# Performance work log

Measured on AMD Instinct MI355X. Metric: run time of the kernel, lower is better.

## Reference

```python
import jax, jax.numpy as jnp
import numpy as np
from jax import lax

EPS = 1e-5

def _instance_norm(x):
    # per-sample, per-channel over HW, affine=False (torch default), biased var
    m = jnp.mean(x, axis=(2, 3), keepdims=True)
    v = jnp.mean((x - m) ** 2, axis=(2, 3), keepdims=True)
    return (x - m) / jnp.sqrt(v + EPS)

def _lrelu(x):
    return jax.nn.leaky_relu(x, 0.2)

def _conv(x, w, b, stride=1, pad=0):
    y = lax.conv_general_dilated(x, w, (stride, stride), ((pad, pad), (pad, pad)),
                                 dimension_numbers=('NCHW', 'OIHW', 'NCHW'))
    return y + b[None, :, None, None]

def _conv_transpose(x, w, b):
    # torch ConvTranspose2d(k=3, stride=2, padding=1, output_padding=1)
    # == dilated conv with lhs_dilation=2, pad (k-1-p, k-1-p+op) = (1, 2),
    # kernel spatially flipped and in/out swapped. w: (Cin, Cout, 3, 3)
    wt = jnp.flip(w, axis=(2, 3)).transpose(1, 0, 2, 3)  # (Cout, Cin, 3, 3)
    y = lax.conv_general_dilated(x, wt, (1, 1), ((1, 2), (1, 2)),
                                 lhs_dilation=(2, 2),
                                 dimension_numbers=('NCHW', 'OIHW', 'NCHW'))
    return y + b[None, :, None, None]

def _reflect_pad1(x):
    return jnp.pad(x, ((0, 0), (0, 0), (1, 1), (1, 1)), mode='reflect')

def _nearest_resize(x, out_h, out_w):
    in_h, in_w = x.shape[2], x.shape[3]
    iy = (jnp.arange(out_h) * (in_h / out_h)).astype(jnp.int32)
    ix = (jnp.arange(out_w) * (in_w / out_w)).astype(jnp.int32)
    return x[:, :, iy][:, :, :, ix]

def setup_inputs() -> dict:
    key = jax.random.key(0)
    ks = jax.random.split(key, 12)
    B, S, H, W = 8, 19, 256, 256
    out_nc = 512
    inp = jax.random.normal(ks[0], (B, 3, H, W), dtype=jnp.float32)
    labels = jax.random.randint(ks[1], (B, 1, H, W), 0, S)
    segmap = (labels == jnp.arange(S).reshape(1, S, 1, 1)).astype(jnp.float32)
    sc = 0.05
    return {
        'input': inp, 'segmap': segmap,
        'w1': jax.random.normal(ks[2], (32, 3, 3, 3), jnp.float32) * sc,
        'b1': jnp.zeros((32,), jnp.float32),
        'w2': jax.random.normal(ks[3], (64, 32, 3, 3), jnp.float32) * sc,
        'b2': jnp.zeros((64,), jnp.float32),
        'w3': jax.random.normal(ks[4], (128, 64, 3, 3), jnp.float32) * sc,
        'b3': jnp.zeros((128,), jnp.float32),
        'w4': jax.random.normal(ks[5], (128, 256, 3, 3), jnp.float32) * sc,  # torch convT layout (Cin, Cout, kh, kw)
        'b4': jnp.zeros((256,), jnp.float32),
        'w5': jax.random.normal(ks[6], (out_nc, 256, 3, 3), jnp.float32) * sc,
        'b5': jnp.zeros((out_nc,), jnp.float32),
    }

def _backbone(x, w1, b1, w2, b2, w3, b3, w4, b4, w5, b5):
    x = _lrelu(_instance_norm(_conv(_reflect_pad1(x), w1, b1)))          # [B,32,256,256]
    x = _lrelu(_instance_norm(_conv(x, w2, b2, stride=2, pad=1)))        # [B,64,128,128]
    x = _lrelu(_instance_norm(_conv(x, w3, b3, stride=2, pad=1)))        # [B,128,64,64]
    x = _lrelu(_instance_norm(_conv_transpose(x, w4, b4)))               # [B,256,128,128]
    x = jnp.tanh(_conv(_reflect_pad1(x), w5, b5))                        # [B,512,128,128]
    return x

def reference(input, segmap, w1, b1, w2, b2, w3, b3, w4, b4, w5, b5):
    codes = _backbone(input, w1, b1, w2, b2, w3, b3, w4, b4, w5, b5)
    seg = _nearest_resize(segmap, codes.shape[2], codes.shape[3])
    mask = (seg > 0).astype(codes.dtype)                                  # segmap.bool()
    sums = jnp.einsum('bchw,bshw->bsc', codes, mask)                      # masked sum per (b, class)
    counts = jnp.sum(mask, axis=(2, 3))[:, :, None]                       # [B,S,1]
    return jnp.where(counts > 0, sums / jnp.maximum(counts, 1.0), 0.0)    # [B,S,C]
```

## Files before the change

### kernel.cpp

```cpp
#include <hip/hip_runtime.h>

#define LB __launch_bounds__(256)

constexpr int S = 19;

typedef __attribute__((ext_vector_type(8))) short frag16;
typedef __attribute__((ext_vector_type(8))) ushort ushort8;
typedef __attribute__((ext_vector_type(4))) float f32x4;

__device__ __forceinline__ int reflect256(int i) { return i < 0 ? -i : (i > 255 ? 510 - i : i); }
__device__ __forceinline__ int reflect128(int i) { return i < 0 ? -i : (i > 127 ? 254 - i : i); }

__device__ __forceinline__ ushort f2bf(float f) {
    union { float f; uint u; } a; a.f = f;
    uint r = a.u + 0x7fffu + ((a.u >> 16) & 1u);
    return (ushort)(r >> 16);
}
__device__ __forceinline__ float bf2f(ushort u) {
    union { uint u; float f; } a; a.u = ((uint)u) << 16; return a.f;
}

__device__ __forceinline__ void gll16(const void* g, void* l) {
    __builtin_amdgcn_global_load_lds(
        (const __attribute__((address_space(1))) void*)g,
        (__attribute__((address_space(3))) void*)l, 16, 0, 0);
}

__global__ LB void k_prep(const float* __restrict__ w2, const float* __restrict__ w3,
                          const float* __restrict__ w4, const float* __restrict__ w5,
                          ushort* __restrict__ t2, ushort* __restrict__ t3,
                          ushort* __restrict__ t4, ushort* __restrict__ t5,
                          float* __restrict__ zf, int ZN) {
    int e = blockIdx.x * 256 + threadIdx.x;
    if (e < ZN) zf[e] = 0.f;
    if (e < 18432) {
        int ci = e & 31, co = (e >> 5) & 63, tap = e >> 11;
        t2[e] = f2bf(w2[(co * 32 + ci) * 9 + tap]);
    } else if (e < 18432 + 73728) {
        int e2 = e - 18432;
        int ci = e2 & 63, co = (e2 >> 6) & 127, tap = e2 >> 13;
        t3[e2] = f2bf(w3[(co * 64 + ci) * 9 + tap]);
    } else if (e < 18432 + 73728 + 294912) {
        int e3 = e - (18432 + 73728);
        int ci = e3 & 127, co = (e3 >> 7) & 255, tap = e3 >> 15;
        t4[e3] = f2bf(w4[ci * 2304 + co * 9 + tap]);
    } else {
        int e4 = e - (18432 + 73728 + 294912);
        int ci = e4 & 255, co = (e4 >> 8) & 511, tap = e4 >> 17;
        t5[e4] = f2bf(w5[(co * 256 + ci) * 9 + tap]);
    }
}

__global__ LB void k_conv1cl(const float* __restrict__ in, const float* __restrict__ w,
                             const float* __restrict__ bias, ushort* __restrict__ out) {
    __shared__ float Wr[864];
    __shared__ float Bs[32];
    int t = threadIdx.x;
    for (int e = t; e < 864; e += 256) Wr[e] = w[e];
    if (t < 32) Bs[t] = bias[t];
    __syncthreads();
    int idx = blockIdx.x * 256 + t;
    int x = idx & 255, y = (idx >> 8) & 255, b = idx >> 16;
    float v[27];
    #pragma unroll
    for (int ci = 0; ci < 3; ++ci) {
        const float* ip = in + ((b * 3 + ci) << 16);
        #pragma unroll
        for (int ky = 0; ky < 3; ++ky) {
            int iy = reflect256(y + ky - 1);
            #pragma unroll
            for (int kx = 0; kx < 3; ++kx) {
                int ix = reflect256(x + kx - 1);
                v[ci * 9 + ky * 3 + kx] = ip[(iy << 8) + ix];
            }
        }
    }
    ushort* op = out + (long)idx * 32;
    #pragma unroll
    for (int g = 0; g < 4; ++g) {
        ushort8 o;
        #pragma unroll
        for (int j = 0; j < 8; ++j) {
            int co = g * 8 + j;
            float a = Bs[co];
            #pragma unroll
            for (int k = 0; k < 27; ++k) a += v[k] * Wr[co * 27 + k];
            o[j] = f2bf(a);
        }
        *(ushort8*)(op + g * 8) = o;
    }
}

template <int C, int PB, int SPLITS>
__global__ LB void k_stats_cl(const ushort* __restrict__ x,
                              float* __restrict__ psum, float* __restrict__ pss) {
    __shared__ float lsum[C], lss[C];
    int b = blockIdx.x / SPLITS, sp = blockIdx.x % SPLITS;
    int t = threadIdx.x;
    if (t < C) { lsum[t] = 0.f; lss[t] = 0.f; }
    __syncthreads();
    constexpr int CG = C / 8;
    constexpr int PO = 256 / CG;
    int c0 = (t % CG) * 8;
    int po = t / CG;
    float s[8], ss[8];
    #pragma unroll
    for (int k = 0; k < 8; ++k) { s[k] = 0.f; ss[k] = 0.f; }
    const ushort* base = x + ((long)b * SPLITS + sp) * (long)PB * C;
    for (int p = po; p < PB; p += PO) {
        ushort8 v = *(const ushort8*)(base + (long)p * C + c0);
        #pragma unroll
        for (int k = 0; k < 8; ++k) {
            float f = bf2f(v[k]);
            s[k] += f; ss[k] += f * f;
        }
    }
    #pragma unroll
    for (int k = 0; k < 8; ++k) {
        atomicAdd(&lsum[c0 + k], s[k]);
        atomicAdd(&lss[c0 + k], ss[k]);
    }
    __syncthreads();
    if (t < C) {
        atomicAdd(&psum[b * C + t], lsum[t]);
        atomicAdd(&pss[b * C + t], lss[t]);
    }
}

template <int C, int P>
__global__ LB void k_nl_cl(ushort* __restrict__ x, const float* __restrict__ psum,
                           const float* __restrict__ pss) {
    __shared__ float M[C], I[C];
    int t = threadIdx.x;
    long e0 = (long)blockIdx.x * 2048;
    int b = (int)(e0 / ((long)P * C));
    if (t < C) {
        float s = psum[b * C + t], q = pss[b * C + t];
        float m = s / (float)P;
        float v = q / (float)P - m * m;
        M[t] = m;
        I[t] = rsqrtf(v + 1e-5f);
    }
    __syncthreads();
    long e = e0 + t * 8;
    int c0 = (int)(e % C);
    ushort8 v = *(ushort8*)(x + e);
    #pragma unroll
    for (int k = 0; k < 8; ++k) {
        float u = (bf2f(v[k]) - M[c0 + k]) * I[c0 + k];
        u = u > 0.f ? u : 0.2f * u;
        v[k] = f2bf(u);
    }
    *(ushort8*)(x + e) = v;
}

__global__ LB void k_conv2m(const ushort* __restrict__ xin, const ushort* __restrict__ wt,
                            const float* __restrict__ bias, ushort* __restrict__ xout) {
    int bx = blockIdx.x;
    int y = bx & 127, b = bx >> 7;
    int t = threadIdx.x, w = t >> 6, lane = t & 63;
    int col0 = w * 32;
    int lanep = lane & 15, hi = lane >> 4;

    f32x4 acc[4][2];
    #pragma unroll
    for (int m = 0; m < 4; ++m)
        #pragma unroll
        for (int n = 0; n < 2; ++n) acc[m][n] = (f32x4){0.f, 0.f, 0.f, 0.f};

    #pragma unroll
    for (int ky = 0; ky < 3; ++ky) {
        int iy = 2 * y + ky - 1;
        if (iy < 0) continue;
        #pragma unroll
        for (int kx = 0; kx < 3; ++kx) {
            int tap = ky * 3 + kx;
            const ushort* wb = wt + ((tap * 64 + lanep) << 5) + hi * 8;
            frag16 av[4];
            #pragma unroll
            for (int m = 0; m < 4; ++m) av[m] = *(const frag16*)(wb + ((m * 16) << 5));
            frag16 bv[2];
            #pragma unroll
            for (int n = 0; n < 2; ++n) {
                int xo = col0 + n * 16 + lanep;
                int ix = 2 * xo + kx - 1;
                frag16 vv = (frag16)(short)0;
                if (ix >= 0)
                    vv = *(const frag16*)(xin + ((((long)(b * 256 + iy)) << 8) + ix) * 32 + hi * 8);
                bv[n] = vv;
            }
            #pragma unroll
            for (int m = 0; m < 4; ++m)
                #pragma unroll
                for (int n = 0; n < 2; ++n)
                    acc[m][n] = __builtin_amdgcn_mfma_f32_16x16x32_bf16(av[m], bv[n], acc[m][n], 0, 0, 0);
        }
    }
    float bvv[4][4];
    #pragma unroll
    for (int m = 0; m < 4; ++m)
        #pragma unroll
        for (int r = 0; r < 4; ++r) bvv[m][r] = bias[m * 16 + hi * 4 + r];
    #pragma unroll
    for (int n = 0; n < 2; ++n) {
        int xo = col0 + n * 16 + lanep;
        long pb = ((((long)(b * 128 + y)) << 7) + xo) * 64 + hi * 4;
        #pragma unroll
        for (int m = 0; m < 4; ++m) {
            ushort4 o;
            o.x = f2bf(acc[m][n][0] + bvv[m][0]);
            o.y = f2bf(acc[m][n][1] + bvv[m][1]);
            o.z = f2bf(acc[m][n][2] + bvv[m][2]);
            o.w = f2bf(acc[m][n][3] + bvv[m][3]);
            *(ushort4*)(xout + pb + m * 16) = o;
        }
    }
}

__global__ LB void k_conv3m(const ushort* __restrict__ xin, const ushort* __restrict__ wt,
                            const float* __restrict__ bias, ushort* __restrict__ xout) {
    int bx = blockIdx.x;
    int y = bx & 63, b = bx >> 6;
    int t = threadIdx.x, w = t >> 6, lane = t & 63;
    int co0 = (w >> 1) * 64;
    int col0 = (w & 1) * 32;
    int lanep = lane & 15, hi = lane >> 4;

    f32x4 acc[4][2];
    #pragma unroll
    for (int m = 0; m < 4; ++m)
        #pragma unroll
        for (int n = 0; n < 2; ++n) acc[m][n] = (f32x4){0.f, 0.f, 0.f, 0.f};

    #pragma unroll
    for (int ky = 0; ky < 3; ++ky) {
        int iy = 2 * y + ky - 1;
        if (iy < 0) continue;
        #pragma unroll
        for (int kx = 0; kx < 3; ++kx) {
            int tap = ky * 3 + kx;
            #pragma unroll
            for (int ck = 0; ck < 2; ++ck) {
                int ci0 = ck * 32;
                const ushort* wb = wt + ((tap * 128 + co0 + lanep) << 6) + ci0 + hi * 8;
                frag16 av[4];
                #pragma unroll
                for (int m = 0; m < 4; ++m) av[m] = *(const frag16*)(wb + ((m * 16) << 6));
                frag16 bv[2];
                #pragma unroll
                for (int n = 0; n < 2; ++n) {
                    int xo = col0 + n * 16 + lanep;
                    int ix = 2 * xo + kx - 1;
                    frag16 vv = (frag16)(short)0;
                    if (ix >= 0)
                        vv = *(const frag16*)(xin + ((((long)(b * 128 + iy)) << 7) + ix) * 64 + ci0 + hi * 8);
                    bv[n] = vv;
                }
                #pragma unroll
                for (int m = 0; m < 4; ++m)
                    #pragma unroll
                    for (int n = 0; n < 2; ++n)
                        acc[m][n] = __builtin_amdgcn_mfma_f32_16x16x32_bf16(av[m], bv[n], acc[m][n], 0, 0, 0);
            }
        }
    }
    float bvv[4][4];
    #pragma unroll
    for (int m = 0; m < 4; ++m)
        #pragma unroll
        for (int r = 0; r < 4; ++r) bvv[m][r] = bias[co0 + m * 16 + hi * 4 + r];
    #pragma unroll
    for (int n = 0; n < 2; ++n) {
        int xo = col0 + n * 16 + lanep;
        long pb = ((((long)(b * 64 + y)) << 6) + xo) * 128 + co0 + hi * 4;
        #pragma unroll
        for (int m = 0; m < 4; ++m) {
            ushort4 o;
            o.x = f2bf(acc[m][n][0] + bvv[m][0]);
            o.y = f2bf(acc[m][n][1] + bvv[m][1]);
            o.z = f2bf(acc[m][n][2] + bvv[m][2]);
            o.w = f2bf(acc[m][n][3] + bvv[m][3]);
            *(ushort4*)(xout + pb + m * 16) = o;
        }
    }
}

__global__ LB void k_convt4m(const ushort* __restrict__ x3l, const ushort* __restrict__ wt,
                             const float* __restrict__ bias, ushort* __restrict__ xl) {
    int bx = blockIdx.x;
    int parity = bx & 3;
    int py = parity >> 1, px = parity & 1;
    int rg = (bx >> 2) & 15;
    int ct = (bx >> 6) & 3;
    int b  = bx >> 8;
    int co0 = ct * 64;
    int t = threadIdx.x;
    int w = t >> 6;
    int ip = rg * 4 + w;
    int lane = t & 63;
    int lanep = lane & 15;
    int hi = lane >> 4;
    int laneq = hi * 8;

    f32x4 acc[4][4];
    #pragma unroll
    for (int m = 0; m < 4; ++m)
        #pragma unroll
        for (int n = 0; n < 4; ++n) acc[m][n] = (f32x4){0.f, 0.f, 0.f, 0.f};

    #pragma unroll
    for (int ky = 0; ky < 3; ++ky) {
        if (((ky + py) & 1) == 0) continue;
        int i = ip + ((py == 1 && ky == 0) ? 1 : 0);
        if (i >= 64) continue;
        #pragma unroll
        for (int kx = 0; kx < 3; ++kx) {
            if (((kx + px) & 1) == 0) continue;
            int dxp = (px == 1 && kx == 0) ? 1 : 0;
            int tap = ky * 3 + kx;
            const ushort* wbase = wt + (((long)tap * 256 + co0 + lanep) << 7) + laneq;
            const ushort* xbase = x3l + ((((long)b << 12) + (i << 6)) << 7) + laneq;
            #pragma unroll
            for (int ci0 = 0; ci0 < 128; ci0 += 32) {
                frag16 av[4], bv[4];
                #pragma unroll
                for (int m = 0; m < 4; ++m)
                    av[m] = *(const frag16*)(wbase + ((m * 16) << 7) + ci0);
                #pragma unroll
                for (int n = 0; n < 4; ++n) {
                    int j = n * 16 + lanep + dxp;
                    bool valid = j < 64;
                    frag16 v = *(const frag16*)(xbase + ((valid ? j : 63) << 7) + ci0);
                    if (!valid) v = (frag16)(short)0;
                    bv[n] = v;
                }
                #pragma unroll
                for (int m = 0; m < 4; ++m)
                    #pragma unroll
                    for (int n = 0; n < 4; ++n)
                        acc[m][n] = __builtin_amdgcn_mfma_f32_16x16x32_bf16(av[m], bv[n], acc[m][n], 0, 0, 0);
            }
        }
    }

    float bvv[4][4];
    #pragma unroll
    for (int m = 0; m < 4; ++m)
        #pragma unroll
        for (int r = 0; r < 4; ++r)
            bvv[m][r] = bias[co0 + m * 16 + hi * 4 + r];
    int y = 2 * ip + py;
    #pragma unroll
    for (int n = 0; n < 4; ++n) {
        int x = 2 * (n * 16 + lanep) + px;
        long pb = ((((long)b << 14) + (y << 7) + x) << 8) + co0 + hi * 4;
        #pragma unroll
        for (int m = 0; m < 4; ++m) {
            ushort4 o;
            o.x = f2bf(acc[m][n][0] + bvv[m][0]);
            o.y = f2bf(acc[m][n][1] + bvv[m][1]);
            o.z = f2bf(acc[m][n][2] + bvv[m][2]);
            o.w = f2bf(acc[m][n][3] + bvv[m][3]);
            *(ushort4*)(xl + pb + m * 16) = o;
        }
    }
}

__global__ LB void k_label(const float* __restrict__ segmap, int* __restrict__ lab,
                           int* __restrict__ counts) {
    __shared__ int h[S];
    if (threadIdx.x < S) h[threadIdx.x] = 0;
    __syncthreads();
    int idx = blockIdx.x * 256 + threadIdx.x;
    int x = idx & 127, y = (idx >> 7) & 127, b = idx >> 14;
    const float* sp = segmap + (long)b * S * 65536 + (y << 1) * 256 + (x << 1);
    int s = 0;
    for (int c = 0; c < S; ++c) {
        if (sp[c * 65536] > 0.f) { s = c; break; }
    }
    lab[idx] = s;
    atomicAdd(&h[s], 1);
    __syncthreads();
    if (threadIdx.x < S) atomicAdd(&counts[b * S + threadIdx.x], h[threadIdx.x]);
}

__global__ void __launch_bounds__(256, 2)
k_conv5m(const ushort* __restrict__ xl, const ushort* __restrict__ wt,
         const float* __restrict__ bias, const int* __restrict__ lab,
         float* __restrict__ sumbuf) {
    __shared__ __align__(16) ushort L[35072];
    float* part = (float*)L;
    constexpr int XS = 0, WS = 16640;

    int bx = blockIdx.x;
    int yp = bx & 63;
    int ct = (bx >> 6) & 7;
    int b  = bx >> 9;
    int y0 = yp * 2, cob = ct * 64;
    int t = threadIdx.x;
    int w = t >> 6;
    int lane = t & 63;
    int row_w = w & 1;
    int col0 = (w >> 1) * 64;
    int lanep = lane & 15;
    int hi = lane >> 4;
    int xw8 = (hi ^ ((lanep >> 1) & 3)) * 8;

    long xbase = (long)b << 14;
    long xg[9]; int wg[9];
    #pragma unroll
    for (int k = 0; k < 9; ++k) {
        int e = t + k * 256;
        int q = e & 3, p = e >> 2;
        int qp = q ^ ((p >> 1) & 3);
        if (e < 2080) {
            int r = p / 130, c = p - r * 130;
            int gy = reflect128(y0 - 1 + r);
            int gc = reflect128(c - 1);
            xg[k] = ((xbase + (gy << 7) + gc) << 8) + qp * 8;
        } else xg[k] = xbase << 8;
        wg[k] = (((p >> 6) * 512 + cob + (p & 63)) << 8) + qp * 8;
    }

    f32x4 acc[4][4];
    #pragma unroll
    for (int m = 0; m < 4; ++m)
        #pragma unroll
        for (int n = 0; n < 4; ++n) acc[m][n] = (f32x4){0.f, 0.f, 0.f, 0.f};

    #pragma unroll 1
    for (int c8 = 0; c8 < 8; ++c8) {
        int cin = c8 * 32;
        #pragma unroll
        for (int k = 0; k < 8; ++k) gll16(xl + xg[k] + cin, L + XS + ((k << 8) + t) * 8);
        if (t < 32) gll16(xl + xg[8] + cin, L + XS + ((8 << 8) + t) * 8);
        #pragma unroll
        for (int k = 0; k < 9; ++k) gll16(wt + wg[k] + cin, L + WS + ((k << 8) + t) * 8);
        __syncthreads();
        #pragma unroll
        for (int tap = 0; tap < 9; ++tap) {
            int ky = tap / 3, kx = tap % 3;
            frag16 av[4];
            #pragma unroll
            for (int m = 0; m < 4; ++m)
                av[m] = *(const frag16*)(L + WS + (tap * 64 + m * 16 + lanep) * 32 + xw8);
            int p0 = (row_w + ky) * 130 + col0 + kx + lanep;
            int bo = p0 * 32 + (hi ^ ((p0 >> 1) & 3)) * 8;
            frag16 bf[4];
            #pragma unroll
            for (int n = 0; n < 4; ++n)
                bf[n] = *(const frag16*)(L + XS + bo + n * 512);
            #pragma unroll
            for (int m = 0; m < 4; ++m)
                #pragma unroll
                for (int n = 0; n < 4; ++n)
                    acc[m][n] = __builtin_amdgcn_mfma_f32_16x16x32_bf16(av[m], bf[n], acc[m][n], 0, 0, 0);
        }
        __syncthreads();
    }

    float bv[4][4];
    #pragma unroll
    for (int m = 0; m < 4; ++m)
        #pragma unroll
        for (int r = 0; r < 4; ++r)
            bv[m][r] = bias[cob + m * 16 + hi * 4 + r];

    for (int e = t; e < S * 64; e += 256) part[e] = 0.f;
    __syncthreads();

    int y = y0 + row_w;
    #pragma unroll
    for (int n = 0; n < 4; ++n) {
        int x = col0 + n * 16 + lanep;
        int s = lab[(b << 14) + (y << 7) + x];
        #pragma unroll
        for (int m = 0; m < 4; ++m)
            #pragma unroll
            for (int r = 0; r < 4; ++r)
                atomicAdd(&part[s * 64 + m * 16 + hi * 4 + r], tanhf(acc[m][n][r] + bv[m][r]));
    }
    __syncthreads();
    for (int e = t; e < S * 64; e += 256) {
        int s = e >> 6, col = e & 63;
        atomicAdd(&sumbuf[((b * S + s) << 9) + cob + col], part[e]);
    }
}

__global__ LB void k_final(const float* __restrict__ sumbuf, const int* __restrict__ counts,
                           float* __restrict__ out) {
    int idx = blockIdx.x * 256 + threadIdx.x;
    int tt = idx >> 9;
    int s = tt % S, b = tt / S;
    int cnt = counts[b * S + s];
    out[idx] = cnt > 0 ? sumbuf[idx] / (float)cnt : 0.f;
}

extern "C" void kernel_launch(void* const* d_in, const int* in_sizes, int n_in,
                              void* d_out, int out_size, void* d_ws, size_t ws_size,
                              hipStream_t stream) {
    const float* input  = (const float*)d_in[0];
    const float* segmap = (const float*)d_in[1];
    const float* w1 = (const float*)d_in[2];  const float* b1 = (const float*)d_in[3];
    const float* w2 = (const float*)d_in[4];  const float* b2 = (const float*)d_in[5];
    const float* w3 = (const float*)d_in[6];  const float* b3 = (const float*)d_in[7];
    const float* w4 = (const float*)d_in[8];  const float* b4 = (const float*)d_in[9];
    const float* w5 = (const float*)d_in[10]; const float* b5 = (const float*)d_in[11];
    float* out = (float*)d_out;

    float* ws = (float*)d_ws;
    ushort* xl    = (ushort*)ws;
    ushort* x1l   = (ushort*)(ws + 16777216);
    ushort* x2l   = (ushort*)(ws + 25165824);
    ushort* x3l   = (ushort*)(ws + 29360128);
    int*   lab    = (int*)(ws + 31539200);
    ushort* wt5   = (ushort*)(ws + 31670528);
    ushort* wt4t  = (ushort*)(ws + 32260352);
    ushort* wt2   = (ushort*)(ws + 32407808);
    ushort* wt3   = (ushort*)(ws + 32417024);
    float* zbase  = ws + 32453888;
    float* sumbuf = zbase;
    int*   counts = (int*)(zbase + 77824);
    float* ps1    = zbase + 78080;
    float* qs1    = zbase + 78336;
    float* ps2    = zbase + 78592;
    float* qs2    = zbase + 79104;
    float* ps3    = zbase + 79616;
    float* qs3    = zbase + 80640;
    float* ps4    = zbase + 81664;
    float* qs4    = zbase + 83712;
    const int ZN  = 85760;

    k_prep<<<6120, 256, 0, stream>>>(w2, w3, w4, w5, wt2, wt3, wt4t, wt5, zbase, ZN);
    k_label<<<512, 256, 0, stream>>>(segmap, lab, counts);
    k_conv1cl<<<2048, 256, 0, stream>>>(input, w1, b1, x1l);
    k_stats_cl<32, 1024, 64><<<512, 256, 0, stream>>>(x1l, ps1, qs1);
    k_nl_cl<32, 65536><<<8192, 256, 0, stream>>>(x1l, ps1, qs1);
    k_conv2m<<<1024, 256, 0, stream>>>(x1l, wt2, b2, x2l);
    k_stats_cl<64, 512, 32><<<256, 256, 0, stream>>>(x2l, ps2, qs2);
    k_nl_cl<64, 16384><<<4096, 256, 0, stream>>>(x2l, ps2, qs2);
    k_conv3m<<<512, 256, 0, stream>>>(x2l, wt3, b3, x3l);
    k_stats_cl<128, 256, 16><<<128, 256, 0, stream>>>(x3l, ps3, qs3);
    k_nl_cl<128, 4096><<<2048, 256, 0, stream>>>(x3l, ps3, qs3);
    k_convt4m<<<2048, 256, 0, stream>>>(x3l, wt4t, b4, xl);
    k_stats_cl<256, 512, 32><<<256, 256, 0, stream>>>(xl, ps4, qs4);
    k_nl_cl<256, 16384><<<16384, 256, 0, stream>>>(xl, ps4, qs4);
    k_conv5m<<<4096, 256, 0, stream>>>(xl, wt5, b5, lab, sumbuf);
    k_final<<<304, 256, 0, stream>>>(sumbuf, counts, out);
}
```

Measured before the change: 891.0 us.

## Load conv5 weights directly into registers and fuse label pass into conv1

In the final conv kernel, the weight tile is no longer staged through LDS. Each lane now loads its MFMA A-fragments for all nine taps straight from global memory into registers, which cuts the LDS footprint roughly in half and removes the LDS weight reads. The price is 36 frag16 registers per thread, a real risk of spills or lower occupancy under launch bounds of (256,2), and uncoalesced per-lane global loads. Separately, the segmap labelling kernel is folded into the first 512 blocks of conv1 to save a launch.

```diff
diff --git a/kernel.cpp b/kernel.cpp
--- a/kernel.cpp
+++ b/kernel.cpp
@@ -52,14 +52,19 @@
 }
 
 __global__ LB void k_conv1cl(const float* __restrict__ in, const float* __restrict__ w,
-                             const float* __restrict__ bias, ushort* __restrict__ out) {
+                             const float* __restrict__ bias, ushort* __restrict__ out,
+                             const float* __restrict__ segmap, int* __restrict__ lab,
+                             int* __restrict__ counts) {
     __shared__ float Wr[864];
     __shared__ float Bs[32];
+    __shared__ int h[S];
     int t = threadIdx.x;
+    int bx = blockIdx.x;
     for (int e = t; e < 864; e += 256) Wr[e] = w[e];
     if (t < 32) Bs[t] = bias[t];
+    if (t < S) h[t] = 0;
     __syncthreads();
-    int idx = blockIdx.x * 256 + t;
+    int idx = bx * 256 + t;
     int x = idx & 255, y = (idx >> 8) & 255, b = idx >> 16;
     float v[27];
     #pragma unroll
@@ -88,6 +93,19 @@
             o[j] = f2bf(a);
         }
         *(ushort8*)(op + g * 8) = o;
+    }
+    if (bx < 512) {
+        int i2 = bx * 256 + t;
+        int lx = i2 & 127, ly = (i2 >> 7) & 127, lb = i2 >> 14;
+        const float* sp = segmap + (long)lb * S * 65536 + (ly << 1) * 256 + (lx << 1);
+        int s = 0;
+        for (int c = 0; c < S; ++c) {
+            if (sp[c * 65536] > 0.f) { s = c; break; }
+        }
+        lab[i2] = s;
+        atomicAdd(&h[s], 1);
+        __syncthreads();
+        if (t < S) atomicAdd(&counts[lb * S + t], h[t]);
     }
 }
 
@@ -366,31 +384,12 @@
     }
 }
 
-__global__ LB void k_label(const float* __restrict__ segmap, int* __restrict__ lab,
-                           int* __restrict__ counts) {
-    __shared__ int h[S];
-    if (threadIdx.x < S) h[threadIdx.x] = 0;
-    __syncthreads();
-    int idx = blockIdx.x * 256 + threadIdx.x;
-    int x = idx & 127, y = (idx >> 7) & 127, b = idx >> 14;
-    const float* sp = segmap + (long)b * S * 65536 + (y << 1) * 256 + (x << 1);
-    int s = 0;
-    for (int c = 0; c < S; ++c) {
-        if (sp[c * 65536] > 0.f) { s = c; break; }
-    }
-    lab[idx] = s;
-    atomicAdd(&h[s], 1);
-    __syncthreads();
-    if (threadIdx.x < S) atomicAdd(&counts[b * S + threadIdx.x], h[threadIdx.x]);
-}
-
 __global__ void __launch_bounds__(256, 2)
 k_conv5m(const ushort* __restrict__ xl, const ushort* __restrict__ wt,
          const float* __restrict__ bias, const int* __restrict__ lab,
          float* __restrict__ sumbuf) {
-    __shared__ __align__(16) ushort L[35072];
+    __shared__ __align__(16) ushort L[16640];
     float* part = (float*)L;
-    constexpr int XS = 0, WS = 16640;
 
     int bx = blockIdx.x;
     int yp = bx & 63;
@@ -404,10 +403,10 @@
     int col0 = (w >> 1) * 64;
     int lanep = lane & 15;
     int hi = lane >> 4;
-    int xw8 = (hi ^ ((lanep >> 1) & 3)) * 8;
+    int laneq = hi * 8;
 
     long xbase = (long)b << 14;
-    long xg[9]; int wg[9];
+    int xg[9];
     #pragma unroll
     for (int k = 0; k < 9; ++k) {
         int e = t + k * 256;
@@ -417,44 +416,48 @@
             int r = p / 130, c = p - r * 130;
             int gy = reflect128(y0 - 1 + r);
             int gc = reflect128(c - 1);
-            xg[k] = ((xbase + (gy << 7) + gc) << 8) + qp * 8;
-        } else xg[k] = xbase << 8;
-        wg[k] = (((p >> 6) * 512 + cob + (p & 63)) << 8) + qp * 8;
-    }
+            xg[k] = (int)(((xbase + (gy << 7) + gc) << 8) + qp * 8);
+        } else xg[k] = (int)(xbase << 8);
+    }
+    int wbo[4];
+    #pragma unroll
+    for (int m = 0; m < 4; ++m)
+        wbo[m] = ((cob + m * 16 + lanep) << 8) + laneq;
 
     f32x4 acc[4][4];
     #pragma unroll
     for (int m = 0; m < 4; ++m)
         #pragma unroll
         for (int n = 0; n < 4; ++n) acc[m][n] = (f32x4){0.f, 0.f, 0.f, 0.f};
+
+    frag16 wr_[9][4];
 
     #pragma unroll 1
     for (int c8 = 0; c8 < 8; ++c8) {
         int cin = c8 * 32;
         #pragma unroll
-        for (int k = 0; k < 8; ++k) gll16(xl + xg[k] + cin, L + XS + ((k << 8) + t) * 8);
-        if (t < 32) gll16(xl + xg[8] + cin, L + XS + ((8 << 8) + t) * 8);
-        #pragma unroll
-        for (int k = 0; k < 9; ++k) gll16(wt + wg[k] + cin, L + WS + ((k << 8) + t) * 8);
+        for (int k = 0; k < 8; ++k) gll16(xl + xg[k] + cin, L + ((k << 8) + t) * 8);
+        if (t < 32) gll16(xl + xg[8] + cin, L + ((8 << 8) + t) * 8);
+        #pragma unroll
+        for (int tap = 0; tap < 9; ++tap)
+            #pragma unroll
+            for (int m = 0; m < 4; ++m)
+                wr_[tap][m] = *(const frag16*)(wt + tap * 131072 + wbo[m] + cin);
         __syncthreads();
         #pragma unroll
         for (int tap = 0; tap < 9; ++tap) {
             int ky = tap / 3, kx = tap % 3;
-            frag16 av[4];
-            #pragma unroll
-            for (int m = 0; m < 4; ++m)
-                av[m] = *(const frag16*)(L + WS + (tap * 64 + m * 16 + lanep) * 32 + xw8);
             int p0 = (row_w + ky) * 130 + col0 + kx + lanep;
             int bo = p0 * 32 + (hi ^ ((p0 >> 1) & 3)) * 8;
             frag16 bf[4];
             #pragma unroll
             for (int n = 0; n < 4; ++n)
-                bf[n] = *(const frag16*)(L + XS + bo + n * 512);
+                bf[n] = *(const frag16*)(L + bo + n * 512);
             #pragma unroll
             for (int m = 0; m < 4; ++m)
                 #pragma unroll
                 for (int n = 0; n < 4; ++n)
-                    acc[m][n] = __builtin_amdgcn_mfma_f32_16x16x32_bf16(av[m], bf[n], acc[m][n], 0, 0, 0);
+                    acc[m][n] = __builtin_amdgcn_mfma_f32_16x16x32_bf16(wr_[tap][m], bf[n], acc[m][n], 0, 0, 0);
         }
         __syncthreads();
     }
@@ -532,8 +535,7 @@
     const int ZN  = 85760;
 
     k_prep<<<6120, 256, 0, stream>>>(w2, w3, w4, w5, wt2, wt3, wt4t, wt5, zbase, ZN);
-    k_label<<<512, 256, 0, stream>>>(segmap, lab, counts);
-    k_conv1cl<<<2048, 256, 0, stream>>>(input, w1, b1, x1l);
+    k_conv1cl<<<2048, 256, 0, stream>>>(input, w1, b1, x1l, segmap, lab, counts);
     k_stats_cl<32, 1024, 64><<<512, 256, 0, stream>>>(x1l, ps1, qs1);
     k_nl_cl<32, 65536><<<8192, 256, 0, stream>>>(x1l, ps1, qs1);
     k_conv2m<<<1024, 256, 0, stream>>>(x1l, wt2, b2, x2l);
```

Measured after the change: 1.210 ms, median of 2. 1.36x slower.
